# Optimization experiments

Hardware: AMD Instinct MI355X
Metric: run time of the kernel (lower is better)

The kernel has to match this reference:

```python
import jax, jax.numpy as jnp
import numpy as np

B, N, D = 8, 2048, 1024  # batch, seq_len, input_dim (= dim_k = dim_v)

def setup_inputs() -> dict:
    key = jax.random.key(0)
    k1, k2, k3, k4, k5 = jax.random.split(key, 5)
    s = 1.0 / np.sqrt(D)
    return {
        "img": jax.random.normal(k1, (B, N, D), dtype=jnp.float32),
        "text": jax.random.normal(k2, (B, N, D), dtype=jnp.float32),
        "Wq": jax.random.normal(k3, (D, D), dtype=jnp.float32) * s,
        "Wk": jax.random.normal(k4, (D, D), dtype=jnp.float32) * s,
        "Wv": jax.random.normal(k5, (D, D), dtype=jnp.float32) * s,
    }

def reference(img, text, Wq, Wk, Wv):
    # Linear layers (bias=False): y = x @ W^T (torch Linear convention)
    Q = jnp.einsum('bnd,kd->bnk', img, Wq)    # [B, N, dim_k]
    K = jnp.einsum('bmd,kd->bmk', text, Wk)   # [B, M, dim_k]
    V = jnp.einsum('bmd,vd->bmv', text, Wv)   # [B, M, dim_v]
    alpha_qk = jnp.einsum('bnk,bmk->bnm', Q, K)  # QK^T, no 1/sqrt(dk) scaling (as in source)
    alpha = jax.nn.softmax(alpha_qk, axis=1)     # softmax over QUERY axis (dim=1), as in source
    out = jnp.einsum('bnm,bmv->bnv', alpha, V)   # [B, N, dim_v]
    feature = out + text
    return (out, feature)
```

## Files before the change

kernel.cpp:

```cpp
#include <hip/hip_runtime.h>
#include <math.h>

#define B 8
#define N 2048
#define D 1024

#define BM 128
#define BN 128
#define BK 32

typedef __bf16 bf16;
typedef __bf16 bf16x8 __attribute__((ext_vector_type(8)));
typedef __bf16 bf16x4 __attribute__((ext_vector_type(4)));
typedef float f32x4 __attribute__((ext_vector_type(4)));

__device__ __forceinline__ void load_lds16(const void* g, void* l) {
    __builtin_amdgcn_global_load_lds((const __attribute__((address_space(1))) void*)g,
                                     (__attribute__((address_space(3))) void*)l, 16, 0, 0);
}

__global__ __launch_bounds__(256) void split_fp32(const float* __restrict__ x,
                                                  bf16* __restrict__ h,
                                                  bf16* __restrict__ l, long n)
{
    long i = ((long)blockIdx.x * 256 + threadIdx.x) * 4;
    if (i >= n) return;
    float4 v = *(const float4*)(x + i);
    float vs[4] = {v.x, v.y, v.z, v.w};
    bf16x4 hh, ll;
#pragma unroll
    for (int t = 0; t < 4; ++t) {
        bf16 hv = (bf16)vs[t];
        hh[t] = hv;
        ll[t] = (bf16)(vs[t] - (float)hv);
    }
    *(bf16x4*)(h + i) = hh;
    *(bf16x4*)(l + i) = ll;
}

__global__ __launch_bounds__(256) void tsplit_1024(const float* __restrict__ W,
                                                   bf16* __restrict__ WT_h,
                                                   bf16* __restrict__ WT_l)
{
    __shared__ float tile[64][65];
    const int d0 = blockIdx.x * 64, k0 = blockIdx.y * 64;
    const int tx = threadIdx.x & 63, ty = threadIdx.x >> 6;
#pragma unroll
    for (int r = 0; r < 16; ++r) {
        int kl = ty + r * 4;
        tile[kl][tx] = W[(size_t)(k0 + kl) * 1024 + d0 + tx];
    }
    __syncthreads();
#pragma unroll
    for (int r = 0; r < 16; ++r) {
        int dl = ty + r * 4;
        float v = tile[tx][dl];
        bf16 hv = (bf16)v;
        size_t idx = (size_t)(d0 + dl) * 1024 + k0 + tx;
        WT_h[idx] = hv;
        WT_l[idx] = (bf16)(v - (float)hv);
    }
}

template<int TERMS, int EPI>
__global__ __launch_bounds__(256) void gemm_nt_mfma(
    const bf16* __restrict__ Ah_g, const bf16* __restrict__ Al_g,
    const bf16* __restrict__ Bh_g, const bf16* __restrict__ Bl_g,
    bf16* __restrict__ Chi, bf16* __restrict__ Clo,
    float* __restrict__ Cf, const float* __restrict__ Text,
    float* __restrict__ Feat,
    int Mdim, int Ncdim, int Kdim, long sA, long sB, long sC)
{
    __shared__ bf16 Ah[BM][BK];
    __shared__ bf16 Bh[BN][BK];
    __shared__ bf16 Al[BM][BK];
    __shared__ bf16 Bl[BN][BK];

    const int tid = threadIdx.x;
    const int lane = tid & 63;
    const int wv = tid >> 6;
    const int wr = (wv >> 1) * 64;
    const int wc = (wv & 1) * 64;
    const int mfrag = lane & 15;
    const int quad = lane >> 4;

    const long z = blockIdx.z;
    const int row0 = blockIdx.y * BM;
    const int col0 = blockIdx.x * BN;

    const bf16* Abh = Ah_g + z * sA;
    const bf16* Abl = (TERMS == 3) ? (Al_g + z * sA) : nullptr;
    const bf16* Bbh = Bh_g + z * sB;
    const bf16* Bbl = (TERMS == 3) ? (Bl_g + z * sB) : nullptr;

    f32x4 acc[4][4] = {};

    for (int k0 = 0; k0 < Kdim; k0 += BK) {
#pragma unroll
        for (int q = 0; q < 2; ++q) {
            int c = q * 256 + tid;
            int row = c >> 2, kp = (c & 3) * 8;
            load_lds16(Abh + (long)(row0 + row) * Kdim + k0 + kp, &Ah[row][kp]);
            load_lds16(Bbh + (long)(col0 + row) * Kdim + k0 + kp, &Bh[row][kp]);
            if constexpr (TERMS == 3) {
                load_lds16(Abl + (long)(row0 + row) * Kdim + k0 + kp, &Al[row][kp]);
                load_lds16(Bbl + (long)(col0 + row) * Kdim + k0 + kp, &Bl[row][kp]);
            }
        }
        __syncthreads();

        bf16x8 a_h[4], b_h[4], a_l[4], b_l[4];
#pragma unroll
        for (int i = 0; i < 4; ++i) {
            a_h[i] = *(const bf16x8*)&Ah[wr + i * 16 + mfrag][quad * 8];
            b_h[i] = *(const bf16x8*)&Bh[wc + i * 16 + mfrag][quad * 8];
            if constexpr (TERMS == 3) {
                a_l[i] = *(const bf16x8*)&Al[wr + i * 16 + mfrag][quad * 8];
                b_l[i] = *(const bf16x8*)&Bl[wc + i * 16 + mfrag][quad * 8];
            }
        }
#pragma unroll
        for (int i = 0; i < 4; ++i)
#pragma unroll
            for (int j = 0; j < 4; ++j) {
                acc[i][j] = __builtin_amdgcn_mfma_f32_16x16x32_bf16(a_h[i], b_h[j], acc[i][j], 0, 0, 0);
                if constexpr (TERMS == 3) {
                    acc[i][j] = __builtin_amdgcn_mfma_f32_16x16x32_bf16(a_h[i], b_l[j], acc[i][j], 0, 0, 0);
                    acc[i][j] = __builtin_amdgcn_mfma_f32_16x16x32_bf16(a_l[i], b_h[j], acc[i][j], 0, 0, 0);
                }
            }
        __syncthreads();
    }

    const long cbase = z * sC;
    const bool wlo = (Clo != nullptr);
#pragma unroll
    for (int i = 0; i < 4; ++i) {
#pragma unroll
        for (int r = 0; r < 4; ++r) {
            int row = row0 + wr + i * 16 + quad * 4 + r;
#pragma unroll
            for (int j = 0; j < 4; ++j) {
                int col = col0 + wc + j * 16 + mfrag;
                long idx = cbase + (long)row * Ncdim + col;
                float v = acc[i][j][r];
                if constexpr (EPI == 0) {
                    bf16 h = (bf16)v;
                    Chi[idx] = h;
                    if (wlo) Clo[idx] = (bf16)(v - (float)h);
                } else if constexpr (EPI == 1) {
                    Cf[idx] = v;
                } else {
                    Cf[idx] = v;
                    Feat[idx] = v + Text[idx];
                }
            }
        }
    }
}

__global__ __launch_bounds__(1024) void col_softmax_bf16(const float* __restrict__ S,
                                                         bf16* __restrict__ Aout)
{
    const int b = blockIdx.x / (N / 64);
    const int mbase = (blockIdx.x % (N / 64)) * 64;
    const int t = threadIdx.x;
    const int mloc = t & 63;
    const int slice = t >> 6;
    const int m = mbase + mloc;
    const float* Sb = S + (size_t)b * N * N;
    bf16* Ab = Aout + (size_t)b * N * N;
    const int n_lo = slice * (N / 16), n_hi = n_lo + (N / 16);

    __shared__ float red_m[16][64];
    __shared__ float red_s[16][64];

    float mx = -INFINITY, s = 0.0f;
    for (int n = n_lo; n < n_hi; n += 8) {
        float x[8];
#pragma unroll
        for (int u = 0; u < 8; ++u) x[u] = Sb[(size_t)(n + u) * N + m];
        float bm = x[0];
#pragma unroll
        for (int u = 1; u < 8; ++u) bm = fmaxf(bm, x[u]);
        float nm = fmaxf(mx, bm);
        float a = 0.0f;
#pragma unroll
        for (int u = 0; u < 8; ++u) a += __expf(x[u] - nm);
        s = s * __expf(mx - nm) + a;
        mx = nm;
    }
    red_m[slice][mloc] = mx;
    red_s[slice][mloc] = s;
    __syncthreads();

    float gm = -INFINITY;
#pragma unroll
    for (int i = 0; i < 16; ++i) gm = fmaxf(gm, red_m[i][mloc]);
    float den = 0.0f;
#pragma unroll
    for (int i = 0; i < 16; ++i) den += red_s[i][mloc] * __expf(red_m[i][mloc] - gm);
    float inv = 1.0f / den;

    for (int n = n_lo; n < n_hi; n += 8) {
        float x[8];
#pragma unroll
        for (int u = 0; u < 8; ++u) x[u] = Sb[(size_t)(n + u) * N + m];
#pragma unroll
        for (int u = 0; u < 8; ++u)
            Ab[(size_t)(n + u) * N + m] = (bf16)(__expf(x[u] - gm) * inv);
    }
}

extern "C" void kernel_launch(void* const* d_in, const int* in_sizes, int n_in,
                              void* d_out, int out_size, void* d_ws, size_t ws_size,
                              hipStream_t stream)
{
    const float* img  = (const float*)d_in[0];
    const float* text = (const float*)d_in[1];
    const float* Wq   = (const float*)d_in[2];
    const float* Wk   = (const float*)d_in[3];
    const float* Wv   = (const float*)d_in[4];

    const long E  = (long)B * N * D;
    const long W2 = (long)D * D;
    const long EN = (long)B * N * N;

    char* ws = (char*)d_ws;
    float* S     = (float*)ws;
    bf16* img_h  = (bf16*)ws;
    bf16* img_l  = img_h + E;
    bf16* WqT_h  = (bf16*)(ws + (size_t)4 * E);
    bf16* WqT_l  = WqT_h + W2;
    bf16* WkT_h  = WqT_l + W2;
    bf16* WkT_l  = WkT_h + W2;
    bf16* Wqk_h  = WkT_l + W2;
    bf16* Wqk_l  = Wqk_h + W2;
    bf16* Wv_l_s = Wqk_l + W2;
    float* out_pv = (float*)ws;

    bf16* text_h = (bf16*)(ws + (size_t)EN * 4);
    bf16* text_l = text_h + E;
    bf16* VT_h   = text_l;

    bf16* T_h  = (bf16*)d_out;
    bf16* T_l  = T_h + E;
    bf16* Wv_h = T_l + E;
    bf16* alpha = (bf16*)d_out;
    float* out  = (float*)d_out;
    float* feat = out + E;

    dim3 blk(256);

    split_fp32<<<E / 1024, blk, 0, stream>>>(img,  img_h,  img_l,  E);
    split_fp32<<<E / 1024, blk, 0, stream>>>(text, text_h, text_l, E);
    split_fp32<<<W2 / 1024, blk, 0, stream>>>(Wv, Wv_h, Wv_l_s, W2);
    tsplit_1024<<<dim3(16, 16), blk, 0, stream>>>(Wq, WqT_h, WqT_l);
    tsplit_1024<<<dim3(16, 16), blk, 0, stream>>>(Wk, WkT_h, WkT_l);

    gemm_nt_mfma<3, 0><<<dim3(8, 8, 1), blk, 0, stream>>>(
        WkT_h, WkT_l, WqT_h, WqT_l, Wqk_h, Wqk_l, nullptr, nullptr, nullptr,
        D, D, D, 0, 0, 0);

    gemm_nt_mfma<3, 0><<<dim3(D / BN, (B * N) / BM, 1), blk, 0, stream>>>(
        img_h, img_l, Wqk_h, Wqk_l, T_h, T_l, nullptr, nullptr, nullptr,
        B * N, D, D, 0, 0, 0);

    gemm_nt_mfma<3, 1><<<dim3(N / BN, N / BM, B), blk, 0, stream>>>(
        T_h, T_l, text_h, text_l, nullptr, nullptr, S, nullptr, nullptr,
        N, N, D, (long)N * D, (long)N * D, (long)N * N);

    gemm_nt_mfma<1, 0><<<dim3(N / BN, D / BM, B), blk, 0, stream>>>(
        Wv_h, nullptr, text_h, nullptr, VT_h, nullptr, nullptr, nullptr, nullptr,
        D, N, D, 0, (long)N * D, (long)D * N);

    col_softmax_bf16<<<dim3(B * N / 64), dim3(1024), 0, stream>>>(S, alpha);

    gemm_nt_mfma<1, 2><<<dim3(D / BN, N / BM, B), blk, 0, stream>>>(
        alpha, nullptr, VT_h, nullptr, nullptr, nullptr, out_pv, text, feat,
        N, D, N, (long)N * N, (long)D * N, (long)N * D);

    hipMemcpyAsync(out, out_pv, (size_t)E * 4, hipMemcpyDeviceToDevice, stream);
}
```

Measured before the change: 920.6 us.

## Replace 128x128 GEMMs with 256x256-tile, 512-thread double-buffered MFMA kernels

Adds two new GEMM kernels, one for the three-term split-bf16 products and one for single-term bf16, that use 256x256 output tiles, 8 waves and double-buffered LDS staging via global_load_lds. The LDS layout is XOR-swizzled to avoid bank conflicts, vmcnt waits are explicit, and s_setprio is raised around the MFMA bursts. The large GEMMs are switched to these kernels, which should raise data reuse per load and overlap global loads with compute. The costs are higher register pressure and LDS use per block, and fewer blocks on some of the grids.

```diff
diff --git a/kernel.cpp b/kernel.cpp
--- a/kernel.cpp
+++ b/kernel.cpp
@@ -18,6 +18,11 @@
     __builtin_amdgcn_global_load_lds((const __attribute__((address_space(1))) void*)g,
                                      (__attribute__((address_space(3))) void*)l, 16, 0, 0);
 }
+
+#define MFMA16(a, b, c) __builtin_amdgcn_mfma_f32_16x16x32_bf16(a, b, c, 0, 0, 0)
+#define BARRIER() asm volatile("s_barrier" ::: "memory")
+#define WAITV8() asm volatile("s_waitcnt vmcnt(8)" ::: "memory")
+#define WAITV0() asm volatile("s_waitcnt vmcnt(0)" ::: "memory")
 
 __global__ __launch_bounds__(256) void split_fp32(const float* __restrict__ x,
                                                   bf16* __restrict__ h,
@@ -123,10 +128,10 @@
         for (int i = 0; i < 4; ++i)
 #pragma unroll
             for (int j = 0; j < 4; ++j) {
-                acc[i][j] = __builtin_amdgcn_mfma_f32_16x16x32_bf16(a_h[i], b_h[j], acc[i][j], 0, 0, 0);
+                acc[i][j] = MFMA16(a_h[i], b_h[j], acc[i][j]);
                 if constexpr (TERMS == 3) {
-                    acc[i][j] = __builtin_amdgcn_mfma_f32_16x16x32_bf16(a_h[i], b_l[j], acc[i][j], 0, 0, 0);
-                    acc[i][j] = __builtin_amdgcn_mfma_f32_16x16x32_bf16(a_l[i], b_h[j], acc[i][j], 0, 0, 0);
+                    acc[i][j] = MFMA16(a_h[i], b_l[j], acc[i][j]);
+                    acc[i][j] = MFMA16(a_l[i], b_h[j], acc[i][j]);
                 }
             }
         __syncthreads();
@@ -159,6 +164,297 @@
     }
 }
 
+
+__device__ __forceinline__ void stage32(const bf16* __restrict__ g, int Kd, int k0,
+                                        bf16* l, int tid)
+{
+#pragma unroll
+    for (int c = 0; c < 2; ++c) {
+        int idx = c * 512 + tid;
+        int row = idx >> 2;
+        int slot = idx & 3;
+        int kk = ((slot ^ ((row >> 1) & 3)) << 3);
+        load_lds16(g + (long)row * Kd + k0 + kk, l + (size_t)idx * 8);
+    }
+}
+
+__device__ __forceinline__ void stage64(const bf16* __restrict__ g, int Kd, int k0,
+                                        bf16* l, int tid)
+{
+#pragma unroll
+    for (int c = 0; c < 4; ++c) {
+        int idx = c * 512 + tid;
+        int row = idx >> 3;
+        int slot = idx & 7;
+        int kk = ((slot ^ (row & 7)) << 3);
+        load_lds16(g + (long)row * Kd + k0 + kk, l + (size_t)idx * 8);
+    }
+}
+
+__device__ __forceinline__ bf16x8 rd32(const bf16* l, int row, int quad) {
+    return *(const bf16x8*)(l + row * 32 + ((quad ^ ((row >> 1) & 3)) << 3));
+}
+__device__ __forceinline__ bf16x8 rd64(const bf16* l, int row, int ks, int quad) {
+    return *(const bf16x8*)(l + row * 64 + (((ks * 4 + quad) ^ (row & 7)) << 3));
+}
+
+template<int EPI>
+__global__ __launch_bounds__(512) void gemm256_3t(
+    const bf16* __restrict__ Ah_g, const bf16* __restrict__ Al_g,
+    const bf16* __restrict__ Bh_g, const bf16* __restrict__ Bl_g,
+    bf16* __restrict__ Chi, bf16* __restrict__ Clo, float* __restrict__ Cf,
+    int Ncdim, int Kdim, long sA, long sB, long sC)
+{
+    __shared__ __align__(16) bf16 lds[2][4][256 * 32];
+
+    const int tid = threadIdx.x;
+    const int lane = tid & 63;
+    const int wv = tid >> 6;
+    const int wrow = (wv >> 2) << 7;
+    const int wcol = (wv & 3) << 6;
+    const int mfrag = lane & 15;
+    const int quad = lane >> 4;
+
+    const long z = blockIdx.z;
+    const int row0 = blockIdx.y * 256;
+    const int col0 = blockIdx.x * 256;
+
+    const bf16* Abh = Ah_g + z * sA + (long)row0 * Kdim;
+    const bf16* Abl = Al_g + z * sA + (long)row0 * Kdim;
+    const bf16* Bbh = Bh_g + z * sB + (long)col0 * Kdim;
+    const bf16* Bbl = Bl_g + z * sB + (long)col0 * Kdim;
+
+    f32x4 acc[8][4] = {};
+    const int NT = Kdim >> 5;
+
+    stage32(Abh, Kdim, 0, lds[0][0], tid);
+    stage32(Abl, Kdim, 0, lds[0][1], tid);
+    stage32(Bbh, Kdim, 0, lds[0][2], tid);
+    stage32(Bbl, Kdim, 0, lds[0][3], tid);
+
+    for (int t = 0; t < NT; ++t) {
+        const int cur = t & 1;
+        const bf16* LAh = lds[cur][0];
+        const bf16* LAl = lds[cur][1];
+        const bf16* LBh = lds[cur][2];
+        const bf16* LBl = lds[cur][3];
+
+        if (t + 1 < NT) {
+            const int k0 = (t + 1) << 5;
+            stage32(Abh, Kdim, k0, lds[cur ^ 1][0], tid);
+            stage32(Abl, Kdim, k0, lds[cur ^ 1][1], tid);
+            stage32(Bbh, Kdim, k0, lds[cur ^ 1][2], tid);
+            stage32(Bbl, Kdim, k0, lds[cur ^ 1][3], tid);
+            WAITV8();
+        } else {
+            WAITV0();
+        }
+        BARRIER();
+        bf16x8 ah[8], bh[4];
+#pragma unroll
+        for (int i = 0; i < 8; ++i) ah[i] = rd32(LAh, wrow + i * 16 + mfrag, quad);
+#pragma unroll
+        for (int j = 0; j < 4; ++j) bh[j] = rd32(LBh, wcol + j * 16 + mfrag, quad);
+        __builtin_amdgcn_s_setprio(1);
+#pragma unroll
+        for (int i = 0; i < 8; ++i)
+#pragma unroll
+            for (int j = 0; j < 4; ++j)
+                acc[i][j] = MFMA16(ah[i], bh[j], acc[i][j]);
+        __builtin_amdgcn_s_setprio(0);
+        BARRIER();
+
+        bf16x8 bl[4];
+#pragma unroll
+        for (int j = 0; j < 4; ++j) bl[j] = rd32(LBl, wcol + j * 16 + mfrag, quad);
+        BARRIER();
+        __builtin_amdgcn_s_setprio(1);
+#pragma unroll
+        for (int i = 0; i < 8; ++i)
+#pragma unroll
+            for (int j = 0; j < 4; ++j)
+                acc[i][j] = MFMA16(ah[i], bl[j], acc[i][j]);
+        __builtin_amdgcn_s_setprio(0);
+        BARRIER();
+
+        bf16x8 al[8];
+#pragma unroll
+        for (int i = 0; i < 8; ++i) al[i] = rd32(LAl, wrow + i * 16 + mfrag, quad);
+        BARRIER();
+        __builtin_amdgcn_s_setprio(1);
+#pragma unroll
+        for (int i = 0; i < 8; ++i)
+#pragma unroll
+            for (int j = 0; j < 4; ++j)
+                acc[i][j] = MFMA16(al[i], bh[j], acc[i][j]);
+        __builtin_amdgcn_s_setprio(0);
+        BARRIER();
+    }
+
+    const long cbase = z * sC;
+    const bool wlo = (Clo != nullptr);
+#pragma unroll
+    for (int i = 0; i < 8; ++i) {
+#pragma unroll
+        for (int r = 0; r < 4; ++r) {
+            int row = row0 + wrow + i * 16 + quad * 4 + r;
+            long rbase = cbase + (long)row * Ncdim;
+#pragma unroll
+            for (int j = 0; j < 4; ++j) {
+                int col = col0 + wcol + j * 16 + mfrag;
+                float v = acc[i][j][r];
+                if constexpr (EPI == 0) {
+                    bf16 h = (bf16)v;
+                    Chi[rbase + col] = h;
+                    if (wlo) Clo[rbase + col] = (bf16)(v - (float)h);
+                } else {
+                    Cf[rbase + col] = v;
+                }
+            }
+        }
+    }
+}
+
+template<int EPI>
+__global__ __launch_bounds__(512) void gemm256_1t(
+    const bf16* __restrict__ A_g, const bf16* __restrict__ B_g,
+    bf16* __restrict__ Chi, float* __restrict__ Cf,
+    const float* __restrict__ Text, float* __restrict__ Feat,
+    int Ncdim, int Kdim, long sA, long sB, long sC)
+{
+    __shared__ __align__(16) bf16 lds[2][2][256 * 64];
+
+    const int tid = threadIdx.x;
+    const int lane = tid & 63;
+    const int wv = tid >> 6;
+    const int wrow = (wv >> 2) << 7;
+    const int wcol = (wv & 3) << 6;
+    const int mfrag = lane & 15;
+    const int quad = lane >> 4;
+
+    const long z = blockIdx.z;
+    const int row0 = blockIdx.y * 256;
+    const int col0 = blockIdx.x * 256;
+
+    const bf16* Ab = A_g + z * sA + (long)row0 * Kdim;
+    const bf16* Bb = B_g + z * sB + (long)col0 * Kdim;
+
+    f32x4 acc[8][4] = {};
+    const int NT = Kdim >> 6;
+
+    stage64(Ab, Kdim, 0, lds[0][0], tid);
+    stage64(Bb, Kdim, 0, lds[0][1], tid);
+
+    for (int t = 0; t < NT; ++t) {
+        const int cur = t & 1;
+        const bf16* LA = lds[cur][0];
+        const bf16* LB = lds[cur][1];
+
+        if (t + 1 < NT) {
+            const int k0 = (t + 1) << 6;
+            stage64(Ab, Kdim, k0, lds[cur ^ 1][0], tid);
+            stage64(Bb, Kdim, k0, lds[cur ^ 1][1], tid);
+            WAITV8();
+        } else {
+            WAITV0();
+        }
+        BARRIER();
+        bf16x8 a[4][2], b0[2][2], b1[2][2];
+#pragma unroll
+        for (int i = 0; i < 4; ++i)
+#pragma unroll
+            for (int ks = 0; ks < 2; ++ks)
+                a[i][ks] = rd64(LA, wrow + i * 16 + mfrag, ks, quad);
+#pragma unroll
+        for (int j = 0; j < 2; ++j)
+#pragma unroll
+            for (int ks = 0; ks < 2; ++ks)
+                b0[j][ks] = rd64(LB, wcol + j * 16 + mfrag, ks, quad);
+        __builtin_amdgcn_s_setprio(1);
+#pragma unroll
+        for (int i = 0; i < 4; ++i)
+#pragma unroll
+            for (int j = 0; j < 2; ++j)
+#pragma unroll
+                for (int ks = 0; ks < 2; ++ks)
+                    acc[i][j] = MFMA16(a[i][ks], b0[j][ks], acc[i][j]);
+        __builtin_amdgcn_s_setprio(0);
+        BARRIER();
+
+#pragma unroll
+        for (int j = 0; j < 2; ++j)
+#pragma unroll
+            for (int ks = 0; ks < 2; ++ks)
+                b1[j][ks] = rd64(LB, wcol + (2 + j) * 16 + mfrag, ks, quad);
+        BARRIER();
+        __builtin_amdgcn_s_setprio(1);
+#pragma unroll
+        for (int i = 0; i < 4; ++i)
+#pragma unroll
+            for (int j = 0; j < 2; ++j)
+#pragma unroll
+                for (int ks = 0; ks < 2; ++ks)
+                    acc[i][2 + j] = MFMA16(a[i][ks], b1[j][ks], acc[i][2 + j]);
+        __builtin_amdgcn_s_setprio(0);
+        BARRIER();
+
+#pragma unroll
+        for (int i = 0; i < 4; ++i)
+#pragma unroll
+            for (int ks = 0; ks < 2; ++ks)
+                a[i][ks] = rd64(LA, wrow + (4 + i) * 16 + mfrag, ks, quad);
+        BARRIER();
+        __builtin_amdgcn_s_setprio(1);
+#pragma unroll
+        for (int i = 0; i < 4; ++i)
+#pragma unroll
+            for (int j = 0; j < 2; ++j)
+#pragma unroll
+                for (int ks = 0; ks < 2; ++ks)
+                    acc[4 + i][2 + j] = MFMA16(a[i][ks], b1[j][ks], acc[4 + i][2 + j]);
+        __builtin_amdgcn_s_setprio(0);
+        BARRIER();
+
+#pragma unroll
+        for (int j = 0; j < 2; ++j)
+#pragma unroll
+            for (int ks = 0; ks < 2; ++ks)
+                b0[j][ks] = rd64(LB, wcol + j * 16 + mfrag, ks, quad);
+        BARRIER();
+        __builtin_amdgcn_s_setprio(1);
+#pragma unroll
+        for (int i = 0; i < 4; ++i)
+#pragma unroll
+            for (int j = 0; j < 2; ++j)
+#pragma unroll
+                for (int ks = 0; ks < 2; ++ks)
+                    acc[4 + i][j] = MFMA16(a[i][ks], b0[j][ks], acc[4 + i][j]);
+        __builtin_amdgcn_s_setprio(0);
+        BARRIER();
+    }
+
+    const long cbase = z * sC;
+#pragma unroll
+    for (int i = 0; i < 8; ++i) {
+#pragma unroll
+        for (int r = 0; r < 4; ++r) {
+            int row = row0 + wrow + i * 16 + quad * 4 + r;
+            long rbase = cbase + (long)row * Ncdim;
+#pragma unroll
+            for (int j = 0; j < 4; ++j) {
+                int col = col0 + wcol + j * 16 + mfrag;
+                float v = acc[i][j][r];
+                if constexpr (EPI == 0) {
+                    Chi[rbase + col] = (bf16)v;
+                } else {
+                    Cf[rbase + col] = v;
+                    Feat[rbase + col] = v + Text[rbase + col];
+                }
+            }
+        }
+    }
+}
+
 __global__ __launch_bounds__(1024) void col_softmax_bf16(const float* __restrict__ S,
                                                          bf16* __restrict__ Aout)
 {
@@ -251,6 +547,7 @@
     float* feat = out + E;
 
     dim3 blk(256);
+    dim3 blk5(512);
 
     split_fp32<<<E / 1024, blk, 0, stream>>>(img,  img_h,  img_l,  E);
     split_fp32<<<E / 1024, blk, 0, stream>>>(text, text_h, text_l, E);
@@ -262,23 +559,23 @@
         WkT_h, WkT_l, WqT_h, WqT_l, Wqk_h, Wqk_l, nullptr, nullptr, nullptr,
         D, D, D, 0, 0, 0);
 
-    gemm_nt_mfma<3, 0><<<dim3(D / BN, (B * N) / BM, 1), blk, 0, stream>>>(
-        img_h, img_l, Wqk_h, Wqk_l, T_h, T_l, nullptr, nullptr, nullptr,
-        B * N, D, D, 0, 0, 0);
-
-    gemm_nt_mfma<3, 1><<<dim3(N / BN, N / BM, B), blk, 0, stream>>>(
-        T_h, T_l, text_h, text_l, nullptr, nullptr, S, nullptr, nullptr,
-        N, N, D, (long)N * D, (long)N * D, (long)N * N);
-
-    gemm_nt_mfma<1, 0><<<dim3(N / BN, D / BM, B), blk, 0, stream>>>(
-        Wv_h, nullptr, text_h, nullptr, VT_h, nullptr, nullptr, nullptr, nullptr,
-        D, N, D, 0, (long)N * D, (long)D * N);
+    gemm256_3t<0><<<dim3(D / 256, (B * N) / 256, 1), blk5, 0, stream>>>(
+        img_h, img_l, Wqk_h, Wqk_l, T_h, T_l, nullptr,
+        D, D, 0, 0, 0);
+
+    gemm256_3t<1><<<dim3(N / 256, N / 256, B), blk5, 0, stream>>>(
+        T_h, T_l, text_h, text_l, nullptr, nullptr, S,
+        N, D, (long)N * D, (long)N * D, (long)N * N);
+
+    gemm256_1t<0><<<dim3(N / 256, D / 256, B), blk5, 0, stream>>>(
+        Wv_h, text_h, VT_h, nullptr, nullptr, nullptr,
+        N, D, 0, (long)N * D, (long)D * N);
 
     col_softmax_bf16<<<dim3(B * N / 64), dim3(1024), 0, stream>>>(S, alpha);
 
-    gemm_nt_mfma<1, 2><<<dim3(D / BN, N / BM, B), blk, 0, stream>>>(
-        alpha, nullptr, VT_h, nullptr, nullptr, nullptr, out_pv, text, feat,
-        N, D, N, (long)N * N, (long)D * N, (long)N * D);
+    gemm256_1t<2><<<dim3(D / 256, N / 256, B), blk5, 0, stream>>>(
+        alpha, VT_h, nullptr, out_pv, text, feat,
+        N * 0 + D, N, (long)N * N, (long)D * N, (long)N * D);
 
     hipMemcpyAsync(out, out_pv, (size_t)E * 4, hipMemcpyDeviceToDevice, stream);
 }
```

Result: faster. 771.3 us (-16.2%).
